# Performance work log

Hardware: AMD Instinct MI355X
Metric: run time of the kernel (lower is better)

## Reference

```python
import jax, jax.numpy as jnp
import numpy as np

B, IN, H, U = 65536, 128, 256, 256

def lecun_tanh(x):
    return 1.7159 * jnp.tanh(0.666 * x)

def _xavier(key, shape):
    fan_out, fan_in = shape
    limit = np.sqrt(6.0 / (fan_in + fan_out))
    return jax.random.uniform(key, shape, jnp.float32, -limit, limit)

def setup_inputs() -> dict:
    key = jax.random.key(0)
    ks = jax.random.split(key, 12)
    return {
        "input": jax.random.normal(ks[0], (B, IN), jnp.float32),
        "hx": jax.random.normal(ks[1], (B, H), jnp.float32),
        "ts": jax.random.uniform(ks[2], (B, 1), jnp.float32),
        # backbone Linear(IN+H -> U)
        "Wb": _xavier(ks[3], (U, IN + H)),
        "bb": jnp.zeros((U,), jnp.float32),
        # ff1, ff2, time_a, time_b: Linear(U -> H)
        "W1": _xavier(ks[4], (H, U)),
        "b1": jnp.zeros((H,), jnp.float32),
        "W2": _xavier(ks[5], (H, U)),
        "b2": jnp.zeros((H,), jnp.float32),
        "Wa": _xavier(ks[6], (H, U)),
        "ba": jnp.zeros((H,), jnp.float32),
        "Wt": _xavier(ks[7], (H, U)),
        "bt": jnp.zeros((H,), jnp.float32),
    }

def reference(input, hx, ts, Wb, bb, W1, b1, W2, b2, Wa, ba, Wt, bt):
    # x = cat([input, hx]) -> backbone MLP (1 layer, LeCun tanh)
    x = jnp.concatenate([input, hx], axis=1)          # [B, IN+H]
    x = lecun_tanh(x @ Wb.T + bb)                     # [B, U]
    ff1 = jnp.tanh(x @ W1.T + b1)                     # [B, H]
    ff2 = jnp.tanh(x @ W2.T + b2)
    t_a = x @ Wa.T + ba
    t_b = x @ Wt.T + bt
    t_interp = jax.nn.sigmoid(t_a * ts + t_b)         # ts broadcasts [B,1]
    new_hidden = ff1 * (1.0 - t_interp) + t_interp * ff2
    return new_hidden
```

## Files before the change

kernel.cpp:

```cpp
#include <hip/hip_runtime.h>

typedef float v4f __attribute__((ext_vector_type(4)));
typedef short v8s __attribute__((ext_vector_type(8)));

#define BM 64

__device__ __forceinline__ unsigned short f2bf(float f) {
    union { float f; unsigned u; } v; v.f = f;
    unsigned u = v.u;
    u += 0x7FFFu + ((u >> 16) & 1u);
    return (unsigned short)(u >> 16);
}

__device__ __forceinline__ unsigned cvt_pk_bf16(float lo, float hi) {
    unsigned r;
    asm("v_cvt_pk_bf16_f32 %0, %1, %2" : "=v"(r) : "v"(lo), "v"(hi));
    return r;
}

#define LDS_BARRIER() do {                                        \
    asm volatile("s_waitcnt lgkmcnt(0)" ::: "memory");            \
    __builtin_amdgcn_s_barrier();                                 \
    __builtin_amdgcn_sched_barrier(0);                            \
} while (0)

#define SB() __builtin_amdgcn_sched_barrier(0)

__device__ __forceinline__ float fast_exp2(float x) {
#if __has_builtin(__builtin_amdgcn_exp2f)
    return __builtin_amdgcn_exp2f(x);
#else
    return exp2f(x);
#endif
}
__device__ __forceinline__ float fast_rcp(float x) {
#if __has_builtin(__builtin_amdgcn_rcpf)
    return __builtin_amdgcn_rcpf(x);
#else
    return 1.0f / x;
#endif
}
__device__ __forceinline__ float fast_tanh(float y) {
    float t = fast_exp2(y * 2.885390081777927f);
    return (t - 1.0f) * fast_rcp(t + 1.0f);
}
__device__ __forceinline__ float fast_sigmoid(float z) {
    float t = fast_exp2(-1.4426950408889634f * z);
    return fast_rcp(1.0f + t);
}

__global__ void prep_pack(const float* __restrict__ Wb, const float* __restrict__ W1,
                          const float* __restrict__ W2, const float* __restrict__ Wa,
                          const float* __restrict__ Wt, unsigned short* __restrict__ ws)
{
    int e = blockIdx.x * 256 + threadIdx.x;
    if (e >= 360448) return;
    const float* src; int K; int base;
    if (e < 98304)       { src = Wb; K = 384; base = 0; }
    else if (e < 163840) { src = W1; K = 256; base = 98304; }
    else if (e < 229376) { src = W2; K = 256; base = 163840; }
    else if (e < 294912) { src = Wa; K = 256; base = 229376; }
    else                 { src = Wt; K = 256; base = 294912; }
    int le   = e - base;
    int j    = le & 7;
    int lane = (le >> 3) & 63;
    int tile = le >> 9;
    int kt   = K >> 5;
    int ks   = tile % kt;
    int nt   = tile / kt;
    int n = nt * 16 + (lane & 15);
    int k = ks * 32 + (lane >> 4) * 8 + j;
    ws[e] = f2bf(src[n * K + k]);
}

__global__ __launch_bounds__(256, 2) void cfc_fused(
    const float* __restrict__ xin, const float* __restrict__ hx,
    const float* __restrict__ ts,
    const float* __restrict__ bb, const float* __restrict__ b1,
    const float* __restrict__ b2, const float* __restrict__ ba,
    const float* __restrict__ bt,
    const unsigned short* __restrict__ wpk,
    float* __restrict__ out)
{
    __shared__ unsigned short lds[16384];
    const int tid  = threadIdx.x;
    const int lane = tid & 63;
    const int w    = tid >> 6;
    const int row0 = blockIdx.x * BM;

    v8s br0[4], br1[4], br2[4];

#define BLOAD(S, DST) do {                                                    \
    _Pragma("unroll")                                                         \
    for (int i = 0; i < 4; ++i) {                                             \
        size_t goff;                                                          \
        if ((S) < 12) {                                                       \
            goff = (size_t)((w * 4 + i) * 12 + (S)) * 512;                    \
        } else {                                                              \
            int s2_ = (S) - 12, g_ = s2_ >> 3, ks_ = s2_ & 7;                 \
            goff = 98304u + (size_t)i * 65536                                 \
                 + (size_t)((w * 4 + g_) * 8 + ks_) * 512;                    \
        }                                                                     \
        DST[i] = *reinterpret_cast<const v8s*>(wpk + goff + (size_t)lane * 8);\
    }                                                                         \
} while (0)

#define ISSUE_IN(SRC, LD, BUF) do {                                           \
    _Pragma("unroll")                                                         \
    for (int it = 0; it < 4; ++it) {                                          \
        int i_ = tid + it * 256; int r_ = i_ >> 4; int c4_ = i_ & 15;         \
        BUF[it] = *(reinterpret_cast<const v4f*>((SRC) + (size_t)r_ * (LD)) + c4_); \
    }                                                                         \
} while (0)

#define WRITE_IN(BUF) do {                                                    \
    _Pragma("unroll")                                                         \
    for (int it = 0; it < 4; ++it) {                                          \
        int i_ = tid + it * 256; int r_ = i_ >> 4; int c4_ = i_ & 15;         \
        uint2 pk_;                                                            \
        pk_.x = cvt_pk_bf16(BUF[it][0], BUF[it][1]);                          \
        pk_.y = cvt_pk_bf16(BUF[it][2], BUF[it][3]);                          \
        int idx_ = (((r_ >> 4) * 2 + (c4_ >> 3)) * 64 + ((c4_ >> 1) & 3) * 16 \
                    + (r_ & 15)) * 8 + (c4_ & 1) * 4;                         \
        *reinterpret_cast<uint2*>(&lds[idx_]) = pk_;                          \
    }                                                                         \
} while (0)

#define P1STEP(S, CUR, PRE) do {                                              \
    BLOAD((S) + 2, PRE);                                                      \
    v8s aa_[4];                                                               \
    _Pragma("unroll")                                                         \
    for (int mt = 0; mt < 4; ++mt)                                            \
        aa_[mt] = *reinterpret_cast<const v8s*>(                              \
                      &lds[((mt * 2 + ((S) & 1)) * 64 + lane) * 8]);          \
    __builtin_amdgcn_s_setprio(1);                                            \
    _Pragma("unroll")                                                         \
    for (int nt = 0; nt < 4; ++nt)                                            \
        _Pragma("unroll")                                                     \
        for (int mt = 0; mt < 4; ++mt)                                        \
            acc[nt][mt] = __builtin_amdgcn_mfma_f32_16x16x32_bf16(            \
                              aa_[mt], CUR[nt], acc[nt][mt], 0, 0, 0);        \
    __builtin_amdgcn_s_setprio(0);                                            \
    SB();                                                                     \
} while (0)

#define P2STEP(S, KS, CUR, PRE) do {                                          \
    BLOAD((S) + 2, PRE);                                                      \
    v8s aa_[4];                                                               \
    _Pragma("unroll")                                                         \
    for (int mt = 0; mt < 4; ++mt)                                            \
        aa_[mt] = *reinterpret_cast<const v8s*>(                              \
                      &lds[((mt * 8 + (KS)) * 64 + lane) * 8]);               \
    __builtin_amdgcn_s_setprio(1);                                            \
    _Pragma("unroll")                                                         \
    for (int mat = 0; mat < 4; ++mat)                                         \
        _Pragma("unroll")                                                     \
        for (int mt = 0; mt < 4; ++mt)                                        \
            a2[mat][mt] = __builtin_amdgcn_mfma_f32_16x16x32_bf16(            \
                              aa_[mt], CUR[mat], a2[mat][mt], 0, 0, 0);       \
    __builtin_amdgcn_s_setprio(0);                                            \
    SB();                                                                     \
} while (0)

#define P2STEP_NS(S, KS, CUR) do {                                            \
    v8s aa_[4];                                                               \
    _Pragma("unroll")                                                         \
    for (int mt = 0; mt < 4; ++mt)                                            \
        aa_[mt] = *reinterpret_cast<const v8s*>(                              \
                      &lds[((mt * 8 + (KS)) * 64 + lane) * 8]);               \
    __builtin_amdgcn_s_setprio(1);                                            \
    _Pragma("unroll")                                                         \
    for (int mat = 0; mat < 4; ++mat)                                         \
        _Pragma("unroll")                                                     \
        for (int mt = 0; mt < 4; ++mt)                                        \
            a2[mat][mt] = __builtin_amdgcn_mfma_f32_16x16x32_bf16(            \
                              aa_[mt], CUR[mat], a2[mat][mt], 0, 0, 0);       \
    __builtin_amdgcn_s_setprio(0);                                            \
    SB();                                                                     \
} while (0)

#define GINIT(G) do {                                                         \
    const int n_ = w * 64 + (G) * 16 + (lane & 15);                           \
    float v1_ = b1[n_], v2_ = b2[n_], va_ = ba[n_], vt_ = bt[n_];             \
    v4f q1_ = {v1_,v1_,v1_,v1_}, q2_ = {v2_,v2_,v2_,v2_};                     \
    v4f qa_ = {va_,va_,va_,va_}, qt_ = {vt_,vt_,vt_,vt_};                     \
    _Pragma("unroll")                                                         \
    for (int mt = 0; mt < 4; ++mt) {                                          \
        a2[0][mt] = q1_; a2[1][mt] = q2_; a2[2][mt] = qa_; a2[3][mt] = qt_;   \
    }                                                                         \
} while (0)

#define EPI(G) do {                                                           \
    const int n_ = w * 64 + (G) * 16 + (lane & 15);                           \
    _Pragma("unroll")                                                         \
    for (int mt = 0; mt < 4; ++mt) {                                          \
        int rowb_ = row0 + mt * 16 + ((lane >> 4) << 2);                      \
        v4f tsv_ = *reinterpret_cast<const v4f*>(&ts[rowb_]);                 \
        _Pragma("unroll")                                                     \
        for (int r = 0; r < 4; ++r) {                                         \
            float ff1_ = fast_tanh(a2[0][mt][r]);                             \
            float ff2_ = fast_tanh(a2[1][mt][r]);                             \
            float ti_  = fast_sigmoid(a2[2][mt][r] * tsv_[r] + a2[3][mt][r]); \
            out[(size_t)(rowb_ + r) * 256 + n_] = ff1_ + ti_ * (ff2_ - ff1_); \
        }                                                                     \
    }                                                                         \
} while (0)

    v4f acc[4][4];
    #pragma unroll
    for (int nt = 0; nt < 4; ++nt) {
        float bv = bb[w * 64 + nt * 16 + (lane & 15)];
        v4f bvv = {bv, bv, bv, bv};
        #pragma unroll
        for (int mt = 0; mt < 4; ++mt) acc[nt][mt] = bvv;
    }

    v4f sA[4], sB[4];
    ISSUE_IN(xin + (size_t)row0 * 128, 128, sA);
    BLOAD(0, br0); BLOAD(1, br1);
    WRITE_IN(sA);
    ISSUE_IN(xin + (size_t)row0 * 128 + 64, 128, sB);
    LDS_BARRIER();
    P1STEP(0, br0, br2); P1STEP(1, br1, br0);
    LDS_BARRIER();
    WRITE_IN(sB);
    ISSUE_IN(hx + (size_t)row0 * 256, 256, sA);
    LDS_BARRIER();
    P1STEP(2, br2, br1); P1STEP(3, br0, br2);
    LDS_BARRIER();
    WRITE_IN(sA);
    ISSUE_IN(hx + (size_t)row0 * 256 + 64, 256, sB);
    LDS_BARRIER();
    P1STEP(4, br1, br0); P1STEP(5, br2, br1);
    LDS_BARRIER();
    WRITE_IN(sB);
    ISSUE_IN(hx + (size_t)row0 * 256 + 128, 256, sA);
    LDS_BARRIER();
    P1STEP(6, br0, br2); P1STEP(7, br1, br0);
    LDS_BARRIER();
    WRITE_IN(sA);
    ISSUE_IN(hx + (size_t)row0 * 256 + 192, 256, sB);
    LDS_BARRIER();
    P1STEP(8, br2, br1); P1STEP(9, br0, br2);
    LDS_BARRIER();
    WRITE_IN(sB);
    LDS_BARRIER();
    P1STEP(10, br1, br0); P1STEP(11, br2, br1);

    LDS_BARRIER();

    #pragma unroll
    for (int nt = 0; nt < 4; ++nt)
        #pragma unroll
        for (int mt = 0; mt < 4; ++mt)
            #pragma unroll
            for (int r = 0; r < 4; ++r) {
                float xv = 1.7159f * fast_tanh(0.666f * acc[nt][mt][r]);
                int idx = ((mt*8 + w*2 + (nt >> 1)) * 64
                           + ((nt & 1)*2 + ((lane >> 3) & 1)) * 16 + (lane >> 4)*4 + r) * 8
                          + (lane & 7);
                lds[idx] = f2bf(xv);
            }
    LDS_BARRIER();

    v4f a2[4][4];
    GINIT(0);
    P2STEP(12,0, br0, br2); P2STEP(13,1, br1, br0);
    P2STEP(14,2, br2, br1); P2STEP(15,3, br0, br2);
    P2STEP(16,4, br1, br0); P2STEP(17,5, br2, br1);
    P2STEP(18,6, br0, br2); P2STEP(19,7, br1, br0);
    EPI(0);
    GINIT(1);
    P2STEP(20,0, br2, br1); P2STEP(21,1, br0, br2);
    P2STEP(22,2, br1, br0); P2STEP(23,3, br2, br1);
    P2STEP(24,4, br0, br2); P2STEP(25,5, br1, br0);
    P2STEP(26,6, br2, br1); P2STEP(27,7, br0, br2);
    EPI(1);
    GINIT(2);
    P2STEP(28,0, br1, br0); P2STEP(29,1, br2, br1);
    P2STEP(30,2, br0, br2); P2STEP(31,3, br1, br0);
    P2STEP(32,4, br2, br1); P2STEP(33,5, br0, br2);
    P2STEP(34,6, br1, br0); P2STEP(35,7, br2, br1);
    EPI(2);
    GINIT(3);
    P2STEP(36,0, br0, br2); P2STEP(37,1, br1, br0);
    P2STEP(38,2, br2, br1); P2STEP(39,3, br0, br2);
    P2STEP(40,4, br1, br0); P2STEP(41,5, br2, br1);
    P2STEP_NS(42,6, br0);   P2STEP_NS(43,7, br1);
    EPI(3);

#undef BLOAD
#undef ISSUE_IN
#undef WRITE_IN
#undef P1STEP
#undef P2STEP
#undef P2STEP_NS
#undef GINIT
#undef EPI
}

extern "C" void kernel_launch(void* const* d_in, const int* in_sizes, int n_in,
                              void* d_out, int out_size, void* d_ws, size_t ws_size,
                              hipStream_t stream)
{
    const float* xin = (const float*)d_in[0];
    const float* hx  = (const float*)d_in[1];
    const float* ts  = (const float*)d_in[2];
    const float* Wb  = (const float*)d_in[3];
    const float* bb  = (const float*)d_in[4];
    const float* W1  = (const float*)d_in[5];
    const float* b1  = (const float*)d_in[6];
    const float* W2  = (const float*)d_in[7];
    const float* b2  = (const float*)d_in[8];
    const float* Wa  = (const float*)d_in[9];
    const float* ba  = (const float*)d_in[10];
    const float* Wt  = (const float*)d_in[11];
    const float* bt  = (const float*)d_in[12];

    if (ws_size < 360448 * sizeof(unsigned short)) return;
    unsigned short* wpk = (unsigned short*)d_ws;

    prep_pack<<<1408, 256, 0, stream>>>(Wb, W1, W2, Wa, Wt, wpk);
    cfc_fused<<<1024, 256, 0, stream>>>(xin, hx, ts, bb, b1, b2, ba, bt, wpk,
                                        (float*)d_out);
}
```

Baseline: 68.40 us.

## Double row tile to 128 so phase-2 weight loads are reused across two halves

Each block now handles 128 rows instead of 64 and launches 512 blocks instead of 1024. The backbone GEMM runs twice, once per 64-row half, into a 4x8 accumulator array. Phase 2 then applies each loaded weight fragment to both halves, which halves the global weight traffic for the four output projections per row. The cost is doubled LDS use (64KB) and about twice the accumulator registers, which may cut occupancy below the 2-blocks-per-CU launch bound or cause spills, and fewer blocks means less parallelism across the GPU.

```diff
diff --git a/kernel.cpp b/kernel.cpp
--- a/kernel.cpp
+++ b/kernel.cpp
@@ -3,7 +3,7 @@
 typedef float v4f __attribute__((ext_vector_type(4)));
 typedef short v8s __attribute__((ext_vector_type(8)));
 
-#define BM 64
+#define BM 128
 
 __device__ __forceinline__ unsigned short f2bf(float f) {
     union { float f; unsigned u; } v; v.f = f;
@@ -82,22 +82,23 @@
     const unsigned short* __restrict__ wpk,
     float* __restrict__ out)
 {
-    __shared__ unsigned short lds[16384];
+    __shared__ unsigned short lds[32768];
     const int tid  = threadIdx.x;
     const int lane = tid & 63;
     const int w    = tid >> 6;
     const int row0 = blockIdx.x * BM;
 
     v8s br0[4], br1[4], br2[4];
+    v4f C[4][8];
 
 #define BLOAD(S, DST) do {                                                    \
     _Pragma("unroll")                                                         \
     for (int i = 0; i < 4; ++i) {                                             \
         size_t goff;                                                          \
-        if ((S) < 12) {                                                       \
-            goff = (size_t)((w * 4 + i) * 12 + (S)) * 512;                    \
+        if ((S) < 24) {                                                       \
+            goff = (size_t)((w * 4 + i) * 12 + ((S) % 12)) * 512;             \
         } else {                                                              \
-            int s2_ = (S) - 12, g_ = s2_ >> 3, ks_ = s2_ & 7;                 \
+            int s2_ = (S) - 24, g_ = s2_ >> 3, ks_ = s2_ & 7;                 \
             goff = 98304u + (size_t)i * 65536                                 \
                  + (size_t)((w * 4 + g_) * 8 + ks_) * 512;                    \
         }                                                                     \
@@ -113,7 +114,7 @@
     }                                                                         \
 } while (0)
 
-#define WRITE_IN(BUF) do {                                                    \
+#define WRITE_IN(BUF, CB) do {                                                \
     _Pragma("unroll")                                                         \
     for (int it = 0; it < 4; ++it) {                                          \
         int i_ = tid + it * 256; int r_ = i_ >> 4; int c4_ = i_ & 15;         \
@@ -122,30 +123,54 @@
         pk_.y = cvt_pk_bf16(BUF[it][2], BUF[it][3]);                          \
         int idx_ = (((r_ >> 4) * 2 + (c4_ >> 3)) * 64 + ((c4_ >> 1) & 3) * 16 \
                     + (r_ & 15)) * 8 + (c4_ & 1) * 4;                         \
-        *reinterpret_cast<uint2*>(&lds[idx_]) = pk_;                          \
-    }                                                                         \
-} while (0)
-
-#define P1STEP(S, CUR, PRE) do {                                              \
+        *reinterpret_cast<uint2*>(&lds[(CB) + idx_]) = pk_;                   \
+    }                                                                         \
+} while (0)
+
+#define ACCINIT(H) do {                                                       \
+    _Pragma("unroll")                                                         \
+    for (int nt = 0; nt < 4; ++nt) {                                          \
+        float bv_ = bb[w * 64 + nt * 16 + (lane & 15)];                       \
+        v4f bq_ = {bv_, bv_, bv_, bv_};                                       \
+        _Pragma("unroll")                                                     \
+        for (int mt = 0; mt < 4; ++mt) C[nt][(H)*4 + mt] = bq_;               \
+    }                                                                         \
+} while (0)
+
+#define P1STEP(S, H, CUR, PRE) do {                                           \
     BLOAD((S) + 2, PRE);                                                      \
     v8s aa_[4];                                                               \
     _Pragma("unroll")                                                         \
     for (int mt = 0; mt < 4; ++mt)                                            \
         aa_[mt] = *reinterpret_cast<const v8s*>(                              \
-                      &lds[((mt * 2 + ((S) & 1)) * 64 + lane) * 8]);          \
+                      &lds[(H)*16384 + ((mt * 2 + ((S) & 1)) * 64 + lane) * 8]); \
     __builtin_amdgcn_s_setprio(1);                                            \
     _Pragma("unroll")                                                         \
     for (int nt = 0; nt < 4; ++nt)                                            \
         _Pragma("unroll")                                                     \
         for (int mt = 0; mt < 4; ++mt)                                        \
-            acc[nt][mt] = __builtin_amdgcn_mfma_f32_16x16x32_bf16(            \
-                              aa_[mt], CUR[nt], acc[nt][mt], 0, 0, 0);        \
+            C[nt][(H)*4 + mt] = __builtin_amdgcn_mfma_f32_16x16x32_bf16(      \
+                              aa_[mt], CUR[nt], C[nt][(H)*4 + mt], 0, 0, 0);  \
     __builtin_amdgcn_s_setprio(0);                                            \
     SB();                                                                     \
 } while (0)
 
-#define P2STEP(S, KS, CUR, PRE) do {                                          \
-    BLOAD((S) + 2, PRE);                                                      \
+#define ACTIVATE(H) do {                                                      \
+    _Pragma("unroll")                                                         \
+    for (int nt = 0; nt < 4; ++nt)                                            \
+        _Pragma("unroll")                                                     \
+        for (int mt = 0; mt < 4; ++mt)                                        \
+            _Pragma("unroll")                                                 \
+            for (int r = 0; r < 4; ++r) {                                     \
+                float xv_ = 1.7159f * fast_tanh(0.666f * C[nt][(H)*4+mt][r]); \
+                int idx_ = ((((H)*4+mt)*8 + w*2 + (nt >> 1)) * 64             \
+                           + ((nt & 1)*2 + ((lane >> 3) & 1)) * 16            \
+                           + (lane >> 4)*4 + r) * 8 + (lane & 7);             \
+                lds[idx_] = f2bf(xv_);                                        \
+            }                                                                 \
+} while (0)
+
+#define P2BODY(KS, CUR) do {                                                  \
     v8s aa_[4];                                                               \
     _Pragma("unroll")                                                         \
     for (int mt = 0; mt < 4; ++mt)                                            \
@@ -156,28 +181,27 @@
     for (int mat = 0; mat < 4; ++mat)                                         \
         _Pragma("unroll")                                                     \
         for (int mt = 0; mt < 4; ++mt)                                        \
-            a2[mat][mt] = __builtin_amdgcn_mfma_f32_16x16x32_bf16(            \
-                              aa_[mt], CUR[mat], a2[mat][mt], 0, 0, 0);       \
+            C[mat][mt] = __builtin_amdgcn_mfma_f32_16x16x32_bf16(             \
+                              aa_[mt], CUR[mat], C[mat][mt], 0, 0, 0);        \
+    __builtin_amdgcn_s_setprio(0);                                            \
+    v8s ab_[4];                                                               \
+    _Pragma("unroll")                                                         \
+    for (int mt = 0; mt < 4; ++mt)                                            \
+        ab_[mt] = *reinterpret_cast<const v8s*>(                              \
+                      &lds[(((mt + 4) * 8 + (KS)) * 64 + lane) * 8]);         \
+    __builtin_amdgcn_s_setprio(1);                                            \
+    _Pragma("unroll")                                                         \
+    for (int mat = 0; mat < 4; ++mat)                                         \
+        _Pragma("unroll")                                                     \
+        for (int mt = 0; mt < 4; ++mt)                                        \
+            C[mat][4 + mt] = __builtin_amdgcn_mfma_f32_16x16x32_bf16(         \
+                              ab_[mt], CUR[mat], C[mat][4 + mt], 0, 0, 0);    \
     __builtin_amdgcn_s_setprio(0);                                            \
     SB();                                                                     \
 } while (0)
 
-#define P2STEP_NS(S, KS, CUR) do {                                            \
-    v8s aa_[4];                                                               \
-    _Pragma("unroll")                                                         \
-    for (int mt = 0; mt < 4; ++mt)                                            \
-        aa_[mt] = *reinterpret_cast<const v8s*>(                              \
-                      &lds[((mt * 8 + (KS)) * 64 + lane) * 8]);               \
-    __builtin_amdgcn_s_setprio(1);                                            \
-    _Pragma("unroll")                                                         \
-    for (int mat = 0; mat < 4; ++mat)                                         \
-        _Pragma("unroll")                                                     \
-        for (int mt = 0; mt < 4; ++mt)                                        \
-            a2[mat][mt] = __builtin_amdgcn_mfma_f32_16x16x32_bf16(            \
-                              aa_[mt], CUR[mat], a2[mat][mt], 0, 0, 0);       \
-    __builtin_amdgcn_s_setprio(0);                                            \
-    SB();                                                                     \
-} while (0)
+#define P2STEP(S, KS, CUR, PRE) do { BLOAD((S) + 2, PRE); P2BODY(KS, CUR); } while (0)
+#define P2STEP_NS(S, KS, CUR)   do { P2BODY(KS, CUR); } while (0)
 
 #define GINIT(G) do {                                                         \
     const int n_ = w * 64 + (G) * 16 + (lane & 15);                           \
@@ -185,114 +209,120 @@
     v4f q1_ = {v1_,v1_,v1_,v1_}, q2_ = {v2_,v2_,v2_,v2_};                     \
     v4f qa_ = {va_,va_,va_,va_}, qt_ = {vt_,vt_,vt_,vt_};                     \
     _Pragma("unroll")                                                         \
-    for (int mt = 0; mt < 4; ++mt) {                                          \
-        a2[0][mt] = q1_; a2[1][mt] = q2_; a2[2][mt] = qa_; a2[3][mt] = qt_;   \
+    for (int mt = 0; mt < 8; ++mt) {                                          \
+        C[0][mt] = q1_; C[1][mt] = q2_; C[2][mt] = qa_; C[3][mt] = qt_;       \
     }                                                                         \
 } while (0)
 
 #define EPI(G) do {                                                           \
     const int n_ = w * 64 + (G) * 16 + (lane & 15);                           \
     _Pragma("unroll")                                                         \
-    for (int mt = 0; mt < 4; ++mt) {                                          \
+    for (int mt = 0; mt < 8; ++mt) {                                          \
         int rowb_ = row0 + mt * 16 + ((lane >> 4) << 2);                      \
         v4f tsv_ = *reinterpret_cast<const v4f*>(&ts[rowb_]);                 \
         _Pragma("unroll")                                                     \
         for (int r = 0; r < 4; ++r) {                                         \
-            float ff1_ = fast_tanh(a2[0][mt][r]);                             \
-            float ff2_ = fast_tanh(a2[1][mt][r]);                             \
-            float ti_  = fast_sigmoid(a2[2][mt][r] * tsv_[r] + a2[3][mt][r]); \
+            float ff1_ = fast_tanh(C[0][mt][r]);                              \
+            float ff2_ = fast_tanh(C[1][mt][r]);                              \
+            float ti_  = fast_sigmoid(C[2][mt][r] * tsv_[r] + C[3][mt][r]);   \
             out[(size_t)(rowb_ + r) * 256 + n_] = ff1_ + ti_ * (ff2_ - ff1_); \
         }                                                                     \
     }                                                                         \
 } while (0)
 
-    v4f acc[4][4];
-    #pragma unroll
-    for (int nt = 0; nt < 4; ++nt) {
-        float bv = bb[w * 64 + nt * 16 + (lane & 15)];
-        v4f bvv = {bv, bv, bv, bv};
-        #pragma unroll
-        for (int mt = 0; mt < 4; ++mt) acc[nt][mt] = bvv;
-    }
-
     v4f sA[4], sB[4];
-    ISSUE_IN(xin + (size_t)row0 * 128, 128, sA);
+    const size_t r0 = (size_t)row0, r1 = (size_t)row0 + 64;
+
+    ISSUE_IN(xin + r0 * 128, 128, sA);
     BLOAD(0, br0); BLOAD(1, br1);
-    WRITE_IN(sA);
-    ISSUE_IN(xin + (size_t)row0 * 128 + 64, 128, sB);
-    LDS_BARRIER();
-    P1STEP(0, br0, br2); P1STEP(1, br1, br0);
-    LDS_BARRIER();
-    WRITE_IN(sB);
-    ISSUE_IN(hx + (size_t)row0 * 256, 256, sA);
-    LDS_BARRIER();
-    P1STEP(2, br2, br1); P1STEP(3, br0, br2);
-    LDS_BARRIER();
-    WRITE_IN(sA);
-    ISSUE_IN(hx + (size_t)row0 * 256 + 64, 256, sB);
-    LDS_BARRIER();
-    P1STEP(4, br1, br0); P1STEP(5, br2, br1);
-    LDS_BARRIER();
-    WRITE_IN(sB);
-    ISSUE_IN(hx + (size_t)row0 * 256 + 128, 256, sA);
-    LDS_BARRIER();
-    P1STEP(6, br0, br2); P1STEP(7, br1, br0);
-    LDS_BARRIER();
-    WRITE_IN(sA);
-    ISSUE_IN(hx + (size_t)row0 * 256 + 192, 256, sB);
-    LDS_BARRIER();
-    P1STEP(8, br2, br1); P1STEP(9, br0, br2);
-    LDS_BARRIER();
-    WRITE_IN(sB);
-    LDS_BARRIER();
-    P1STEP(10, br1, br0); P1STEP(11, br2, br1);
-
-    LDS_BARRIER();
-
-    #pragma unroll
-    for (int nt = 0; nt < 4; ++nt)
-        #pragma unroll
-        for (int mt = 0; mt < 4; ++mt)
-            #pragma unroll
-            for (int r = 0; r < 4; ++r) {
-                float xv = 1.7159f * fast_tanh(0.666f * acc[nt][mt][r]);
-                int idx = ((mt*8 + w*2 + (nt >> 1)) * 64
-                           + ((nt & 1)*2 + ((lane >> 3) & 1)) * 16 + (lane >> 4)*4 + r) * 8
-                          + (lane & 7);
-                lds[idx] = f2bf(xv);
-            }
-    LDS_BARRIER();
-
-    v4f a2[4][4];
+    ACCINIT(0);
+    WRITE_IN(sA, 0);
+    ISSUE_IN(xin + r0 * 128 + 64, 128, sB);
+    LDS_BARRIER();
+    P1STEP(0,0, br0, br2); P1STEP(1,0, br1, br0);
+    LDS_BARRIER();
+    WRITE_IN(sB, 0); ISSUE_IN(hx + r0 * 256, 256, sA);
+    LDS_BARRIER();
+    P1STEP(2,0, br2, br1); P1STEP(3,0, br0, br2);
+    LDS_BARRIER();
+    WRITE_IN(sA, 0); ISSUE_IN(hx + r0 * 256 + 64, 256, sB);
+    LDS_BARRIER();
+    P1STEP(4,0, br1, br0); P1STEP(5,0, br2, br1);
+    LDS_BARRIER();
+    WRITE_IN(sB, 0); ISSUE_IN(hx + r0 * 256 + 128, 256, sA);
+    LDS_BARRIER();
+    P1STEP(6,0, br0, br2); P1STEP(7,0, br1, br0);
+    LDS_BARRIER();
+    WRITE_IN(sA, 0); ISSUE_IN(hx + r0 * 256 + 192, 256, sB);
+    LDS_BARRIER();
+    P1STEP(8,0, br2, br1); P1STEP(9,0, br0, br2);
+    LDS_BARRIER();
+    WRITE_IN(sB, 0); ISSUE_IN(xin + r1 * 128, 128, sA);
+    LDS_BARRIER();
+    P1STEP(10,0, br1, br0); P1STEP(11,0, br2, br1);
+    LDS_BARRIER();
+    ACTIVATE(0);
+    ACCINIT(1);
+    WRITE_IN(sA, 16384); ISSUE_IN(xin + r1 * 128 + 64, 128, sB);
+    LDS_BARRIER();
+
+    P1STEP(12,1, br0, br2); P1STEP(13,1, br1, br0);
+    LDS_BARRIER();
+    WRITE_IN(sB, 16384); ISSUE_IN(hx + r1 * 256, 256, sA);
+    LDS_BARRIER();
+    P1STEP(14,1, br2, br1); P1STEP(15,1, br0, br2);
+    LDS_BARRIER();
+    WRITE_IN(sA, 16384); ISSUE_IN(hx + r1 * 256 + 64, 256, sB);
+    LDS_BARRIER();
+    P1STEP(16,1, br1, br0); P1STEP(17,1, br2, br1);
+    LDS_BARRIER();
+    WRITE_IN(sB, 16384); ISSUE_IN(hx + r1 * 256 + 128, 256, sA);
+    LDS_BARRIER();
+    P1STEP(18,1, br0, br2); P1STEP(19,1, br1, br0);
+    LDS_BARRIER();
+    WRITE_IN(sA, 16384); ISSUE_IN(hx + r1 * 256 + 192, 256, sB);
+    LDS_BARRIER();
+    P1STEP(20,1, br2, br1); P1STEP(21,1, br0, br2);
+    LDS_BARRIER();
+    WRITE_IN(sB, 16384);
+    LDS_BARRIER();
+    P1STEP(22,1, br1, br0); P1STEP(23,1, br2, br1);
+    LDS_BARRIER();
+    ACTIVATE(1);
+    LDS_BARRIER();
+
     GINIT(0);
-    P2STEP(12,0, br0, br2); P2STEP(13,1, br1, br0);
-    P2STEP(14,2, br2, br1); P2STEP(15,3, br0, br2);
-    P2STEP(16,4, br1, br0); P2STEP(17,5, br2, br1);
-    P2STEP(18,6, br0, br2); P2STEP(19,7, br1, br0);
+    P2STEP(24,0, br0, br2); P2STEP(25,1, br1, br0);
+    P2STEP(26,2, br2, br1); P2STEP(27,3, br0, br2);
+    P2STEP(28,4, br1, br0); P2STEP(29,5, br2, br1);
+    P2STEP(30,6, br0, br2); P2STEP(31,7, br1, br0);
     EPI(0);
     GINIT(1);
-    P2STEP(20,0, br2, br1); P2STEP(21,1, br0, br2);
-    P2STEP(22,2, br1, br0); P2STEP(23,3, br2, br1);
-    P2STEP(24,4, br0, br2); P2STEP(25,5, br1, br0);
-    P2STEP(26,6, br2, br1); P2STEP(27,7, br0, br2);
+    P2STEP(32,0, br2, br1); P2STEP(33,1, br0, br2);
+    P2STEP(34,2, br1, br0); P2STEP(35,3, br2, br1);
+    P2STEP(36,4, br0, br2); P2STEP(37,5, br1, br0);
+    P2STEP(38,6, br2, br1); P2STEP(39,7, br0, br2);
     EPI(1);
     GINIT(2);
-    P2STEP(28,0, br1, br0); P2STEP(29,1, br2, br1);
-    P2STEP(30,2, br0, br2); P2STEP(31,3, br1, br0);
-    P2STEP(32,4, br2, br1); P2STEP(33,5, br0, br2);
-    P2STEP(34,6, br1, br0); P2STEP(35,7, br2, br1);
+    P2STEP(40,0, br1, br0); P2STEP(41,1, br2, br1);
+    P2STEP(42,2, br0, br2); P2STEP(43,3, br1, br0);
+    P2STEP(44,4, br2, br1); P2STEP(45,5, br0, br2);
+    P2STEP(46,6, br1, br0); P2STEP(47,7, br2, br1);
     EPI(2);
     GINIT(3);
-    P2STEP(36,0, br0, br2); P2STEP(37,1, br1, br0);
-    P2STEP(38,2, br2, br1); P2STEP(39,3, br0, br2);
-    P2STEP(40,4, br1, br0); P2STEP(41,5, br2, br1);
-    P2STEP_NS(42,6, br0);   P2STEP_NS(43,7, br1);
+    P2STEP(48,0, br0, br2); P2STEP(49,1, br1, br0);
+    P2STEP(50,2, br2, br1); P2STEP(51,3, br0, br2);
+    P2STEP(52,4, br1, br0); P2STEP(53,5, br2, br1);
+    P2STEP_NS(54,6, br0);   P2STEP_NS(55,7, br1);
     EPI(3);
 
 #undef BLOAD
 #undef ISSUE_IN
 #undef WRITE_IN
+#undef ACCINIT
 #undef P1STEP
+#undef ACTIVATE
+#undef P2BODY
 #undef P2STEP
 #undef P2STEP_NS
 #undef GINIT
@@ -321,6 +351,6 @@
     unsigned short* wpk = (unsigned short*)d_ws;
 
     prep_pack<<<1408, 256, 0, stream>>>(Wb, W1, W2, Wa, Wt, wpk);
-    cfc_fused<<<1024, 256, 0, stream>>>(xin, hx, ts, bb, b1, b2, ba, bt, wpk,
-                                        (float*)d_out);
-}
+    cfc_fused<<<512, 256, 0, stream>>>(xin, hx, ts, bb, b1, b2, ba, bt, wpk,
+                                       (float*)d_out);
+}
```

After: 92.73 us. 35.6% more time.

## Load phase-1 A operands directly from global into MFMA registers, bypassing LDS

Applied to the files above, without the earlier changes.

Phase 1 no longer stages input/hx tiles through LDS. Each wave loads its A fragments straight from global memory in the MFMA operand layout, converts them to bf16 in registers, and prefetches the next K step's fragments one step ahead. This removes the LDS writes, LDS reads and the many block barriers around phase 1. In exchange, every one of the four waves now reads the same A rows redundantly from global/L2, with 32-byte per-lane strided accesses that coalesce less well. It also holds 8 more v4f registers live, which adds register pressure at launch_bounds(256,2).

```diff
diff --git a/kernel.cpp b/kernel.cpp
--- a/kernel.cpp
+++ b/kernel.cpp
@@ -2,6 +2,7 @@
 
 typedef float v4f __attribute__((ext_vector_type(4)));
 typedef short v8s __attribute__((ext_vector_type(8)));
+typedef unsigned v4u __attribute__((ext_vector_type(4)));
 
 #define BM 64
 
@@ -89,6 +90,7 @@
     const int row0 = blockIdx.x * BM;
 
     v8s br0[4], br1[4], br2[4];
+    v4f fA[8];
 
 #define BLOAD(S, DST) do {                                                    \
     _Pragma("unroll")                                                         \
@@ -105,34 +107,36 @@
     }                                                                         \
 } while (0)
 
-#define ISSUE_IN(SRC, LD, BUF) do {                                           \
-    _Pragma("unroll")                                                         \
-    for (int it = 0; it < 4; ++it) {                                          \
-        int i_ = tid + it * 256; int r_ = i_ >> 4; int c4_ = i_ & 15;         \
-        BUF[it] = *(reinterpret_cast<const v4f*>((SRC) + (size_t)r_ * (LD)) + c4_); \
-    }                                                                         \
-} while (0)
-
-#define WRITE_IN(BUF) do {                                                    \
-    _Pragma("unroll")                                                         \
-    for (int it = 0; it < 4; ++it) {                                          \
-        int i_ = tid + it * 256; int r_ = i_ >> 4; int c4_ = i_ & 15;         \
-        uint2 pk_;                                                            \
-        pk_.x = cvt_pk_bf16(BUF[it][0], BUF[it][1]);                          \
-        pk_.y = cvt_pk_bf16(BUF[it][2], BUF[it][3]);                          \
-        int idx_ = (((r_ >> 4) * 2 + (c4_ >> 3)) * 64 + ((c4_ >> 1) & 3) * 16 \
-                    + (r_ & 15)) * 8 + (c4_ & 1) * 4;                         \
-        *reinterpret_cast<uint2*>(&lds[idx_]) = pk_;                          \
+#define AISSUE(S) do {                                                        \
+    const float* src_; int ld_, kb_;                                          \
+    if ((S) < 4) { src_ = xin; ld_ = 128; kb_ = (S) * 32; }                   \
+    else         { src_ = hx;  ld_ = 256; kb_ = ((S) - 4) * 32; }             \
+    _Pragma("unroll")                                                         \
+    for (int mt = 0; mt < 4; ++mt) {                                          \
+        const float* b_ = src_ + (size_t)(row0 + mt * 16 + (lane & 15)) * ld_ \
+                          + kb_ + ((lane >> 4) << 3);                         \
+        fA[2 * mt]     = *reinterpret_cast<const v4f*>(b_);                   \
+        fA[2 * mt + 1] = *reinterpret_cast<const v4f*>(b_ + 4);               \
+    }                                                                         \
+} while (0)
+
+#define ACVT(AA) do {                                                         \
+    _Pragma("unroll")                                                         \
+    for (int mt = 0; mt < 4; ++mt) {                                          \
+        v4u tu_;                                                              \
+        tu_[0] = cvt_pk_bf16(fA[2*mt][0],   fA[2*mt][1]);                     \
+        tu_[1] = cvt_pk_bf16(fA[2*mt][2],   fA[2*mt][3]);                     \
+        tu_[2] = cvt_pk_bf16(fA[2*mt+1][0], fA[2*mt+1][1]);                   \
+        tu_[3] = cvt_pk_bf16(fA[2*mt+1][2], fA[2*mt+1][3]);                   \
+        AA[mt] = *reinterpret_cast<v8s*>(&tu_);                               \
     }                                                                         \
 } while (0)
 
 #define P1STEP(S, CUR, PRE) do {                                              \
+    v8s aa_[4];                                                               \
+    ACVT(aa_);                                                                \
+    if ((S) < 11) AISSUE((S) + 1);                                            \
     BLOAD((S) + 2, PRE);                                                      \
-    v8s aa_[4];                                                               \
-    _Pragma("unroll")                                                         \
-    for (int mt = 0; mt < 4; ++mt)                                            \
-        aa_[mt] = *reinterpret_cast<const v8s*>(                              \
-                      &lds[((mt * 2 + ((S) & 1)) * 64 + lane) * 8]);          \
     __builtin_amdgcn_s_setprio(1);                                            \
     _Pragma("unroll")                                                         \
     for (int nt = 0; nt < 4; ++nt)                                            \
@@ -215,39 +219,15 @@
         for (int mt = 0; mt < 4; ++mt) acc[nt][mt] = bvv;
     }
 
-    v4f sA[4], sB[4];
-    ISSUE_IN(xin + (size_t)row0 * 128, 128, sA);
+    AISSUE(0);
     BLOAD(0, br0); BLOAD(1, br1);
-    WRITE_IN(sA);
-    ISSUE_IN(xin + (size_t)row0 * 128 + 64, 128, sB);
-    LDS_BARRIER();
-    P1STEP(0, br0, br2); P1STEP(1, br1, br0);
-    LDS_BARRIER();
-    WRITE_IN(sB);
-    ISSUE_IN(hx + (size_t)row0 * 256, 256, sA);
-    LDS_BARRIER();
-    P1STEP(2, br2, br1); P1STEP(3, br0, br2);
-    LDS_BARRIER();
-    WRITE_IN(sA);
-    ISSUE_IN(hx + (size_t)row0 * 256 + 64, 256, sB);
-    LDS_BARRIER();
-    P1STEP(4, br1, br0); P1STEP(5, br2, br1);
-    LDS_BARRIER();
-    WRITE_IN(sB);
-    ISSUE_IN(hx + (size_t)row0 * 256 + 128, 256, sA);
-    LDS_BARRIER();
-    P1STEP(6, br0, br2); P1STEP(7, br1, br0);
-    LDS_BARRIER();
-    WRITE_IN(sA);
-    ISSUE_IN(hx + (size_t)row0 * 256 + 192, 256, sB);
-    LDS_BARRIER();
-    P1STEP(8, br2, br1); P1STEP(9, br0, br2);
-    LDS_BARRIER();
-    WRITE_IN(sB);
-    LDS_BARRIER();
+
+    P1STEP(0, br0, br2);  P1STEP(1, br1, br0);
+    P1STEP(2, br2, br1);  P1STEP(3, br0, br2);
+    P1STEP(4, br1, br0);  P1STEP(5, br2, br1);
+    P1STEP(6, br0, br2);  P1STEP(7, br1, br0);
+    P1STEP(8, br2, br1);  P1STEP(9, br0, br2);
     P1STEP(10, br1, br0); P1STEP(11, br2, br1);
-
-    LDS_BARRIER();
 
     #pragma unroll
     for (int nt = 0; nt < 4; ++nt)
@@ -290,8 +270,8 @@
     EPI(3);
 
 #undef BLOAD
-#undef ISSUE_IN
-#undef WRITE_IN
+#undef AISSUE
+#undef ACVT
 #undef P1STEP
 #undef P2STEP
 #undef P2STEP_NS
```

New measurement: 93.88 us. 1.37x slower.

## Double-buffer phase-2 accumulators to overlap epilogue with next group's MFMAs

Applied to the files above, without the earlier changes.

Phase 2 now uses two accumulator sets, even and odd. The epilogue of one output group is split into per-row-tile chunks and interleaved with the MFMA steps of the next group, so tanh/sigmoid math and global stores overlap matrix work instead of stalling it. To make room for the extra 64 accumulator registers, the phase-1 input staging drops its second buffer and reuses one. The added register pressure could cause spills or lower occupancy, and the single staging buffer serializes input loads more tightly.

```diff
diff --git a/kernel.cpp b/kernel.cpp
--- a/kernel.cpp
+++ b/kernel.cpp
@@ -144,7 +144,7 @@
     SB();                                                                     \
 } while (0)
 
-#define P2STEP(S, KS, CUR, PRE) do {                                          \
+#define P2STEP(S, KS, CUR, PRE, A2) do {                                      \
     BLOAD((S) + 2, PRE);                                                      \
     v8s aa_[4];                                                               \
     _Pragma("unroll")                                                         \
@@ -156,13 +156,13 @@
     for (int mat = 0; mat < 4; ++mat)                                         \
         _Pragma("unroll")                                                     \
         for (int mt = 0; mt < 4; ++mt)                                        \
-            a2[mat][mt] = __builtin_amdgcn_mfma_f32_16x16x32_bf16(            \
-                              aa_[mt], CUR[mat], a2[mat][mt], 0, 0, 0);       \
+            A2[mat][mt] = __builtin_amdgcn_mfma_f32_16x16x32_bf16(            \
+                              aa_[mt], CUR[mat], A2[mat][mt], 0, 0, 0);       \
     __builtin_amdgcn_s_setprio(0);                                            \
     SB();                                                                     \
 } while (0)
 
-#define P2STEP_NS(S, KS, CUR) do {                                            \
+#define P2STEP_NS(S, KS, CUR, A2) do {                                        \
     v8s aa_[4];                                                               \
     _Pragma("unroll")                                                         \
     for (int mt = 0; mt < 4; ++mt)                                            \
@@ -173,37 +173,38 @@
     for (int mat = 0; mat < 4; ++mat)                                         \
         _Pragma("unroll")                                                     \
         for (int mt = 0; mt < 4; ++mt)                                        \
-            a2[mat][mt] = __builtin_amdgcn_mfma_f32_16x16x32_bf16(            \
-                              aa_[mt], CUR[mat], a2[mat][mt], 0, 0, 0);       \
+            A2[mat][mt] = __builtin_amdgcn_mfma_f32_16x16x32_bf16(            \
+                              aa_[mt], CUR[mat], A2[mat][mt], 0, 0, 0);       \
     __builtin_amdgcn_s_setprio(0);                                            \
     SB();                                                                     \
 } while (0)
 
-#define GINIT(G) do {                                                         \
+#define GINIT(G, A2) do {                                                     \
     const int n_ = w * 64 + (G) * 16 + (lane & 15);                           \
     float v1_ = b1[n_], v2_ = b2[n_], va_ = ba[n_], vt_ = bt[n_];             \
     v4f q1_ = {v1_,v1_,v1_,v1_}, q2_ = {v2_,v2_,v2_,v2_};                     \
     v4f qa_ = {va_,va_,va_,va_}, qt_ = {vt_,vt_,vt_,vt_};                     \
     _Pragma("unroll")                                                         \
     for (int mt = 0; mt < 4; ++mt) {                                          \
-        a2[0][mt] = q1_; a2[1][mt] = q2_; a2[2][mt] = qa_; a2[3][mt] = qt_;   \
-    }                                                                         \
-} while (0)
-
-#define EPI(G) do {                                                           \
+        A2[0][mt] = q1_; A2[1][mt] = q2_; A2[2][mt] = qa_; A2[3][mt] = qt_;   \
+    }                                                                         \
+} while (0)
+
+#define EPIMT(G, A2, MT) do {                                                 \
     const int n_ = w * 64 + (G) * 16 + (lane & 15);                           \
-    _Pragma("unroll")                                                         \
-    for (int mt = 0; mt < 4; ++mt) {                                          \
-        int rowb_ = row0 + mt * 16 + ((lane >> 4) << 2);                      \
-        v4f tsv_ = *reinterpret_cast<const v4f*>(&ts[rowb_]);                 \
-        _Pragma("unroll")                                                     \
-        for (int r = 0; r < 4; ++r) {                                         \
-            float ff1_ = fast_tanh(a2[0][mt][r]);                             \
-            float ff2_ = fast_tanh(a2[1][mt][r]);                             \
-            float ti_  = fast_sigmoid(a2[2][mt][r] * tsv_[r] + a2[3][mt][r]); \
-            out[(size_t)(rowb_ + r) * 256 + n_] = ff1_ + ti_ * (ff2_ - ff1_); \
-        }                                                                     \
-    }                                                                         \
+    int rowb_ = row0 + (MT) * 16 + ((lane >> 4) << 2);                        \
+    v4f tsv_ = *reinterpret_cast<const v4f*>(&ts[rowb_]);                     \
+    _Pragma("unroll")                                                         \
+    for (int r = 0; r < 4; ++r) {                                             \
+        float ff1_ = fast_tanh(A2[0][(MT)][r]);                               \
+        float ff2_ = fast_tanh(A2[1][(MT)][r]);                               \
+        float ti_  = fast_sigmoid(A2[2][(MT)][r] * tsv_[r] + A2[3][(MT)][r]); \
+        out[(size_t)(rowb_ + r) * 256 + n_] = ff1_ + ti_ * (ff2_ - ff1_);     \
+    }                                                                         \
+} while (0)
+
+#define EPI(G, A2) do {                                                       \
+    EPIMT(G, A2, 0); EPIMT(G, A2, 1); EPIMT(G, A2, 2); EPIMT(G, A2, 3);       \
 } while (0)
 
     v4f acc[4][4];
@@ -215,35 +216,35 @@
         for (int mt = 0; mt < 4; ++mt) acc[nt][mt] = bvv;
     }
 
-    v4f sA[4], sB[4];
+    v4f sA[4];
     ISSUE_IN(xin + (size_t)row0 * 128, 128, sA);
     BLOAD(0, br0); BLOAD(1, br1);
     WRITE_IN(sA);
-    ISSUE_IN(xin + (size_t)row0 * 128 + 64, 128, sB);
+    ISSUE_IN(xin + (size_t)row0 * 128 + 64, 128, sA);
     LDS_BARRIER();
     P1STEP(0, br0, br2); P1STEP(1, br1, br0);
     LDS_BARRIER();
-    WRITE_IN(sB);
+    WRITE_IN(sA);
     ISSUE_IN(hx + (size_t)row0 * 256, 256, sA);
     LDS_BARRIER();
     P1STEP(2, br2, br1); P1STEP(3, br0, br2);
     LDS_BARRIER();
     WRITE_IN(sA);
-    ISSUE_IN(hx + (size_t)row0 * 256 + 64, 256, sB);
+    ISSUE_IN(hx + (size_t)row0 * 256 + 64, 256, sA);
     LDS_BARRIER();
     P1STEP(4, br1, br0); P1STEP(5, br2, br1);
     LDS_BARRIER();
-    WRITE_IN(sB);
+    WRITE_IN(sA);
     ISSUE_IN(hx + (size_t)row0 * 256 + 128, 256, sA);
     LDS_BARRIER();
     P1STEP(6, br0, br2); P1STEP(7, br1, br0);
     LDS_BARRIER();
     WRITE_IN(sA);
-    ISSUE_IN(hx + (size_t)row0 * 256 + 192, 256, sB);
+    ISSUE_IN(hx + (size_t)row0 * 256 + 192, 256, sA);
     LDS_BARRIER();
     P1STEP(8, br2, br1); P1STEP(9, br0, br2);
     LDS_BARRIER();
-    WRITE_IN(sB);
+    WRITE_IN(sA);
     LDS_BARRIER();
     P1STEP(10, br1, br0); P1STEP(11, br2, br1);
 
@@ -263,31 +264,41 @@
             }
     LDS_BARRIER();
 
-    v4f a2[4][4];
-    GINIT(0);
-    P2STEP(12,0, br0, br2); P2STEP(13,1, br1, br0);
-    P2STEP(14,2, br2, br1); P2STEP(15,3, br0, br2);
-    P2STEP(16,4, br1, br0); P2STEP(17,5, br2, br1);
-    P2STEP(18,6, br0, br2); P2STEP(19,7, br1, br0);
-    EPI(0);
-    GINIT(1);
-    P2STEP(20,0, br2, br1); P2STEP(21,1, br0, br2);
-    P2STEP(22,2, br1, br0); P2STEP(23,3, br2, br1);
-    P2STEP(24,4, br0, br2); P2STEP(25,5, br1, br0);
-    P2STEP(26,6, br2, br1); P2STEP(27,7, br0, br2);
-    EPI(1);
-    GINIT(2);
-    P2STEP(28,0, br1, br0); P2STEP(29,1, br2, br1);
-    P2STEP(30,2, br0, br2); P2STEP(31,3, br1, br0);
-    P2STEP(32,4, br2, br1); P2STEP(33,5, br0, br2);
-    P2STEP(34,6, br1, br0); P2STEP(35,7, br2, br1);
-    EPI(2);
-    GINIT(3);
-    P2STEP(36,0, br0, br2); P2STEP(37,1, br1, br0);
-    P2STEP(38,2, br2, br1); P2STEP(39,3, br0, br2);
-    P2STEP(40,4, br1, br0); P2STEP(41,5, br2, br1);
-    P2STEP_NS(42,6, br0);   P2STEP_NS(43,7, br1);
-    EPI(3);
+    v4f a2E[4][4], a2O[4][4];
+
+    GINIT(0, a2E);
+    P2STEP(12,0, br0, br2, a2E); P2STEP(13,1, br1, br0, a2E);
+    P2STEP(14,2, br2, br1, a2E); P2STEP(15,3, br0, br2, a2E);
+    P2STEP(16,4, br1, br0, a2E); P2STEP(17,5, br2, br1, a2E);
+    P2STEP(18,6, br0, br2, a2E); P2STEP(19,7, br1, br0, a2E);
+    GINIT(1, a2O);
+    P2STEP(20,0, br2, br1, a2O); EPIMT(0, a2E, 0);
+    P2STEP(21,1, br0, br2, a2O);
+    P2STEP(22,2, br1, br0, a2O); EPIMT(0, a2E, 1);
+    P2STEP(23,3, br2, br1, a2O);
+    P2STEP(24,4, br0, br2, a2O); EPIMT(0, a2E, 2);
+    P2STEP(25,5, br1, br0, a2O);
+    P2STEP(26,6, br2, br1, a2O); EPIMT(0, a2E, 3);
+    P2STEP(27,7, br0, br2, a2O);
+    GINIT(2, a2E);
+    P2STEP(28,0, br1, br0, a2E); EPIMT(1, a2O, 0);
+    P2STEP(29,1, br2, br1, a2E);
+    P2STEP(30,2, br0, br2, a2E); EPIMT(1, a2O, 1);
+    P2STEP(31,3, br1, br0, a2E);
+    P2STEP(32,4, br2, br1, a2E); EPIMT(1, a2O, 2);
+    P2STEP(33,5, br0, br2, a2E);
+    P2STEP(34,6, br1, br0, a2E); EPIMT(1, a2O, 3);
+    P2STEP(35,7, br2, br1, a2E);
+    GINIT(3, a2O);
+    P2STEP(36,0, br0, br2, a2O); EPIMT(2, a2E, 0);
+    P2STEP(37,1, br1, br0, a2O);
+    P2STEP(38,2, br2, br1, a2O); EPIMT(2, a2E, 1);
+    P2STEP(39,3, br0, br2, a2O);
+    P2STEP(40,4, br1, br0, a2O); EPIMT(2, a2E, 2);
+    P2STEP(41,5, br2, br1, a2O);
+    P2STEP_NS(42,6, br0, a2O);   EPIMT(2, a2E, 3);
+    P2STEP_NS(43,7, br1, a2O);
+    EPI(3, a2O);
 
 #undef BLOAD
 #undef ISSUE_IN
@@ -296,6 +307,7 @@
 #undef P2STEP
 #undef P2STEP_NS
 #undef GINIT
+#undef EPIMT
 #undef EPI
 }
 
```

Result: slower. 75.10 us (+9.8%).
